# Kernel optimization log

Hardware: AMD Instinct MI355X
Metric: run time of the kernel (lower is better)

Reference implementation:

```python
import jax, jax.numpy as jnp
import numpy as np

FEAT_STRIDE = 16
POOL = 7
POST_NMS = 300
NUM_ANCHORS = 9
SCALES = np.array([8.0, 16.0, 32.0])
RATIOS = np.array([0.5, 1.0, 2.0])


def _base_anchors():
    w = h = 16.0
    xc = yc = 7.5
    size = w * h
    ws = np.round(np.sqrt(size / RATIOS))
    hs = np.round(ws * RATIOS)
    ratio_anchors = np.stack([xc - 0.5 * (ws - 1), yc - 0.5 * (hs - 1),
                              xc + 0.5 * (ws - 1), yc + 0.5 * (hs - 1)], 1)
    out = []
    for a in ratio_anchors:
        aw = a[2] - a[0] + 1.0
        ah = a[3] - a[1] + 1.0
        acx = a[0] + 0.5 * (aw - 1)
        acy = a[1] + 0.5 * (ah - 1)
        ws_ = aw * SCALES
        hs_ = ah * SCALES
        out.append(np.stack([acx - 0.5 * (ws_ - 1), acy - 0.5 * (hs_ - 1),
                             acx + 0.5 * (ws_ - 1), acy + 0.5 * (hs_ - 1)], 1))
    return np.concatenate(out, 0)  # [9,4]


def _all_anchors(H, W):
    base = _base_anchors()
    sx = np.arange(W) * FEAT_STRIDE
    sy = np.arange(H) * FEAT_STRIDE
    gx, gy = np.meshgrid(sx, sy)  # [H,W], x fastest -> matches NHWC flatten
    shifts = np.stack([gx.ravel(), gy.ravel(), gx.ravel(), gy.ravel()], 1)
    return jnp.asarray((shifts[:, None, :] + base[None, :, :]).reshape(-1, 4),
                       jnp.float32)  # [H*W*9, 4]


def _conv(x, w, b, pad):
    y = jax.lax.conv_general_dilated(x, w, (1, 1), [(pad, pad), (pad, pad)],
                                     dimension_numbers=('NCHW', 'OIHW', 'NCHW'))
    return y + b[None, :, None, None]


def _affine_grid(theta, H, W):
    # torch affine_grid, align_corners=True (torch<=1.2 default)
    xs = jnp.linspace(-1.0, 1.0, W)
    ys = jnp.linspace(-1.0, 1.0, H)
    gx, gy = jnp.meshgrid(xs, ys)
    base = jnp.stack([gx, gy, jnp.ones_like(gx)], -1)  # [H,W,3]
    return jnp.einsum('nij,hwj->nhwi', theta, base)  # [N,H,W,2] (x,y)


def _bilinear(img, x, y):
    # img [C,H,W]; x,y [h,w] pixel coords; zeros padding, align_corners=True
    H, W = img.shape[1], img.shape[2]
    x0 = jnp.floor(x)
    y0 = jnp.floor(y)
    x1 = x0 + 1.0
    y1 = y0 + 1.0
    wx1 = x - x0
    wx0 = 1.0 - wx1
    wy1 = y - y0
    wy0 = 1.0 - wy1

    def g(xi, yi):
        xc = jnp.clip(xi, 0, W - 1).astype(jnp.int32)
        yc = jnp.clip(yi, 0, H - 1).astype(jnp.int32)
        valid = ((xi >= 0) & (xi <= W - 1) & (yi >= 0) & (yi <= H - 1))
        return img[:, yc, xc] * valid.astype(img.dtype)

    return (g(x0, y0) * (wx0 * wy0) + g(x1, y0) * (wx1 * wy0)
            + g(x0, y1) * (wx0 * wy1) + g(x1, y1) * (wx1 * wy1))


def _pix(grid, H, W):
    x = (grid[..., 0] + 1.0) * 0.5 * (W - 1)
    y = (grid[..., 1] + 1.0) * 0.5 * (H - 1)
    return x, y


def strpn_forward(head_features, im_info, w_rpn, b_rpn, w_cls, b_cls,
                  w_bbox, b_bbox, w_trans, b_trans):
    H, W = head_features.shape[2], head_features.shape[3]
    anchors = _all_anchors(H, W)

    rpn = jax.nn.relu(_conv(head_features, w_rpn, b_rpn, 1))
    cls = _conv(rpn, w_cls, b_cls, 0)      # [1,18,H,W]
    bbox = _conv(rpn, w_bbox, b_bbox, 0)   # [1,36,H,W]
    trans = _conv(rpn, w_trans, b_trans, 0)  # [1,54,H,W]

    # view(1,2,9*H,W) softmax over dim1: channels 0..8=bg, 9..17=fg
    prob = jax.nn.softmax(cls.reshape(1, 2, NUM_ANCHORS, H, W), axis=1)[:, 1]
    scores = prob.transpose(0, 2, 3, 1).reshape(-1)          # [H*W*9]
    deltas = bbox.transpose(0, 2, 3, 1).reshape(-1, 4)
    tparam = trans.transpose(0, 2, 3, 1).reshape(-1, 6)

    # bbox_transform_inv
    aw = anchors[:, 2] - anchors[:, 0] + 1.0
    ah = anchors[:, 3] - anchors[:, 1] + 1.0
    acx = anchors[:, 0] + 0.5 * aw
    acy = anchors[:, 1] + 0.5 * ah
    pcx = deltas[:, 0] * aw + acx
    pcy = deltas[:, 1] * ah + acy
    pw = jnp.exp(deltas[:, 2]) * aw
    ph = jnp.exp(deltas[:, 3]) * ah
    x1 = jnp.clip(pcx - 0.5 * pw, 0.0, im_info[1] - 1.0)
    y1 = jnp.clip(pcy - 0.5 * ph, 0.0, im_info[0] - 1.0)
    x2 = jnp.clip(pcx + 0.5 * pw, 0.0, im_info[1] - 1.0)
    y2 = jnp.clip(pcy + 0.5 * ph, 0.0, im_info[0] - 1.0)

    # proposal selection: fixed-size top-K by fg score (NMS elided, see notes)
    _, idx = jax.lax.top_k(scores, POST_NMS)
    boxes = jnp.stack([x1, y1, x2, y2], 1)[idx]              # [300,4]
    tsel = tparam[idx]                                       # [300,6]
    rois = jnp.concatenate(
        [jnp.zeros((POST_NMS, 1), boxes.dtype), boxes], 1)   # [300,5]

    # affine-grid ROI pooling (STRPN.pooling, max_pool=True)
    fx1 = boxes[:, 0] / 16.0
    fy1 = boxes[:, 1] / 16.0
    fx2 = boxes[:, 2] / 16.0
    fy2 = boxes[:, 3] / 16.0
    Wf = jnp.float32(W)
    Hf = jnp.float32(H)
    t00 = (fx2 - fx1) / (Wf - 1)
    t02 = (fx1 + fx2 - Wf + 1) / (Wf - 1)
    t11 = (fy2 - fy1) / (Hf - 1)
    t12 = (fy1 + fy2 - Hf + 1) / (Hf - 1)
    z = jnp.zeros_like(t00)
    theta = jnp.stack([jnp.stack([t00, z, t02], -1),
                       jnp.stack([z, t11, t12], -1)], 1)     # [300,2,3]

    pre = 2 * POOL
    grid = _affine_grid(theta, pre, pre)
    xg, yg = _pix(grid, H, W)
    img = head_features[0]
    crops = jax.vmap(_bilinear, in_axes=(None, 0, 0))(img, xg, yg)  # [300,C,14,14]
    N, C = crops.shape[0], crops.shape[1]
    pooled = crops.reshape(N, C, POOL, 2, POOL, 2).max(axis=(3, 5))  # [300,C,7,7]

    # spatial transform with predicted per-ROI affine params
    theta2 = tsel.reshape(-1, 2, 3)
    grid2 = _affine_grid(theta2, POOL, POOL)
    x2g, y2g = _pix(grid2, POOL, POOL)
    transformed = jax.vmap(_bilinear)(pooled, x2g, y2g)       # [300,C,7,7]
    return rois, pooled, transformed


def setup_inputs() -> dict:
    key = jax.random.key(0)
    ks = jax.random.split(key, 10)
    C_in, C_rpn = 1024, 512
    inp = {
        'head_features': jax.random.normal(ks[0], (1, C_in, 50, 75), jnp.float32),
        'gt_boxes': jax.random.uniform(ks[1], (5, 5), jnp.float32) * 100.0,
        'im_info': jnp.array([800.0, 1200.0, 1.0], jnp.float32),
        'w_rpn': jax.random.normal(ks[2], (C_rpn, C_in, 3, 3), jnp.float32) * 0.01,
        'b_rpn': jnp.zeros((C_rpn,), jnp.float32),
        'w_cls': jax.random.normal(ks[3], (2 * NUM_ANCHORS, C_rpn, 1, 1), jnp.float32) * 0.01,
        'b_cls': jnp.zeros((2 * NUM_ANCHORS,), jnp.float32),
        'w_bbox': jax.random.normal(ks[4], (4 * NUM_ANCHORS, C_rpn, 1, 1), jnp.float32) * 0.01,
        'b_bbox': jnp.zeros((4 * NUM_ANCHORS,), jnp.float32),
        'w_trans': jax.random.normal(ks[5], (6 * NUM_ANCHORS, C_rpn, 1, 1), jnp.float32) * 0.01,
        'b_trans': jnp.zeros((6 * NUM_ANCHORS,), jnp.float32),
    }
    return inp


def reference(head_features, gt_boxes, im_info, w_rpn, b_rpn, w_cls, b_cls,
              w_bbox, b_bbox, w_trans, b_trans):
    # gt_boxes is unused in the inference 'gallery' path (kept for signature parity)
    return strpn_forward(head_features, im_info, w_rpn, b_rpn, w_cls, b_cls,
                         w_bbox, b_bbox, w_trans, b_trans)
```

## Files before the change

### kernel.cpp

```cpp
#include <hip/hip_runtime.h>
#include <hip/hip_bf16.h>
#include <stdint.h>

typedef unsigned int u32;
typedef unsigned long long u64;

#define HH 50
#define WW 75
#define NPOS 3750
#define NANCH 33750
#define CAP 4096
#define RPSZ 1920000

__constant__ float c_aw[9] = {184.f,368.f,736.f,128.f,256.f,512.f,88.f,176.f,352.f};
__constant__ float c_ah[9] = {96.f,192.f,384.f,128.f,256.f,512.f,176.f,352.f,704.f};

__global__ __launch_bounds__(256) void k_tw2(const float* __restrict__ w, float* __restrict__ wTb) {
  __shared__ __align__(16) float T[72*129];
  int tile = blockIdx.x;
  int ch   = blockIdx.y;
  int ocb = tile >> 2, ks = tile & 3;
  int t = threadIdx.x;
  const float* src = w + (size_t)(ocb*128)*9216 + (size_t)(ks*256 + ch*8)*9;
  #pragma unroll
  for (int i = 0; i < 36; ++i) {
    int e = t + i*256;
    int oc = e / 72, f = e - oc*72;
    T[f*129 + oc] = src[(size_t)oc*9216 + f];
  }
  __syncthreads();
  float* dst = wTb + ((size_t)tile*32 + ch)*9216;
  #pragma unroll
  for (int i = 0; i < 9; ++i) {
    int j = t + i*256;
    int f = j >> 5, o4 = (j & 31)*4;
    float4 v = make_float4(T[f*129+o4], T[f*129+o4+1], T[f*129+o4+2], T[f*129+o4+3]);
    *(float4*)&dst[(size_t)j*4] = v;
  }
}

__global__ __launch_bounds__(256) void k_tf(const float* __restrict__ head, float* __restrict__ fT) {
  __shared__ float tile[32][33];
  int p0 = blockIdx.x*32, c0 = blockIdx.y*32;
  int tx = threadIdx.x & 31, ty = threadIdx.x >> 5;
  #pragma unroll
  for (int k = 0; k < 4; ++k) {
    int cc = c0 + ty + k*8, pp = p0 + tx;
    tile[ty + k*8][tx] = (pp < NPOS) ? head[(size_t)cc*NPOS + pp] : 0.f;
  }
  __syncthreads();
  #pragma unroll
  for (int k = 0; k < 4; ++k) {
    int pp = p0 + ty + k*8, cc = c0 + tx;
    if (pp < NPOS) fT[(size_t)pp*1024 + cc] = tile[tx][ty + k*8];
  }
}

__global__ __launch_bounds__(256) void k_conv(const float* __restrict__ head,
                                              const float* __restrict__ wTb,
                                              float* __restrict__ rpnP) {
  __shared__ __align__(16) float Ws[9216];
  __shared__ __align__(16) float Xs[8*6*80 + 16];
  int ocb = blockIdx.x;
  int ks  = blockIdx.z;
  int t = threadIdx.x;
  int lane = t & 63;
  int g = blockIdx.y*4 + (t >> 6);
  if (g >= 125) g = 124;
  int rp  = __builtin_amdgcn_readfirstlane(g / 5);
  int sub = __builtin_amdgcn_readfirstlane(g - (g/5)*5);
  int rpA = (int)((blockIdx.y*4) / 5);
  int x0 = sub * 16;
  int rbase = 2*rpA - 1;
  int rloc = 2*(rp - rpA);

  float a00[16], a01[16], a10[16], a11[16];
  #pragma unroll
  for (int j = 0; j < 16; ++j) { a00[j]=0.f; a01[j]=0.f; a10[j]=0.f; a11[j]=0.f; }

  const float* wsrc = wTb + (size_t)(ocb*4 + ks)*32*9216;
  int ic0 = ks*256;

  #pragma unroll 1
  for (int ch = 0; ch < 32; ++ch) {
    #pragma unroll
    for (int i = 0; i < 9; ++i) {
      int e = t + i*256;
      *(float4*)&Ws[e*4] = *(const float4*)(wsrc + (size_t)ch*9216 + (size_t)e*4);
    }
    int icc = ic0 + ch*8;
    #pragma unroll
    for (int i = 0; i < 15; ++i) {
      int e = t + i*256;
      int il = e / 480; int r = e - il*480;
      int rr = r / 80;  int xx = r - rr*80;
      int sy = rbase + rr, sx = xx - 1;
      float v = 0.f;
      if (sy >= 0 && sy < HH && sx >= 0 && sx < WW)
        v = head[(size_t)(icc + il)*NPOS + sy*WW + sx];
      Xs[e] = v;
    }
    __syncthreads();
    #pragma unroll 1
    for (int il = 0; il < 8; ++il) {
      float wv0[9], wv1[9];
      #pragma unroll
      for (int k = 0; k < 9; ++k) {
        float2 w2 = *(const float2*)&Ws[(il*9 + k)*128 + 2*lane];
        wv0[k] = w2.x; wv1[k] = w2.y;
      }
      const float* xbase = &Xs[(il*6 + rloc)*80 + x0];
      #pragma unroll
      for (int ri = 0; ri < 4; ++ri) {
        float4 q0 = *(const float4*)(xbase + ri*80);
        float4 q1 = *(const float4*)(xbase + ri*80 + 4);
        float4 q2 = *(const float4*)(xbase + ri*80 + 8);
        float4 q3 = *(const float4*)(xbase + ri*80 + 12);
        float4 q4 = *(const float4*)(xbase + ri*80 + 16);
        float sxv[20] = {q0.x,q0.y,q0.z,q0.w, q1.x,q1.y,q1.z,q1.w,
                         q2.x,q2.y,q2.z,q2.w, q3.x,q3.y,q3.z,q3.w,
                         q4.x,q4.y,q4.z,q4.w};
        if (ri < 3) {
          #pragma unroll
          for (int kx = 0; kx < 3; ++kx) {
            float w0 = wv0[ri*3+kx], w1 = wv1[ri*3+kx];
            #pragma unroll
            for (int j = 0; j < 16; ++j) {
              a00[j] = fmaf(w0, sxv[j+kx], a00[j]);
              a01[j] = fmaf(w1, sxv[j+kx], a01[j]);
            }
          }
        }
        if (ri > 0) {
          #pragma unroll
          for (int kx = 0; kx < 3; ++kx) {
            float w0 = wv0[(ri-1)*3+kx], w1 = wv1[(ri-1)*3+kx];
            #pragma unroll
            for (int j = 0; j < 16; ++j) {
              a10[j] = fmaf(w0, sxv[j+kx], a10[j]);
              a11[j] = fmaf(w1, sxv[j+kx], a11[j]);
            }
          }
        }
      }
    }
    __syncthreads();
  }
  float* outp = rpnP + (size_t)ks*RPSZ;
  int ocl = ocb*128 + 2*lane;
  int or0 = 2*rp;
  #pragma unroll
  for (int j = 0; j < 16; ++j) {
    int x = x0 + j;
    if (x < WW) {
      *(float2*)&outp[(size_t)(or0*WW + x)*512 + ocl]     = make_float2(a00[j], a01[j]);
      *(float2*)&outp[(size_t)((or0+1)*WW + x)*512 + ocl] = make_float2(a10[j], a11[j]);
    }
  }
}

__global__ __launch_bounds__(256) void k_cls(const float* __restrict__ rp,
    const float* __restrict__ brpn,
    const float* __restrict__ w_cls, const float* __restrict__ b_cls,
    const float* __restrict__ w_bbox, const float* __restrict__ b_bbox,
    const float* __restrict__ w_tr, const float* __restrict__ b_tr,
    const float* __restrict__ iminfo,
    u32* __restrict__ sk, float* __restrict__ boxes, float* __restrict__ tpar) {
  __shared__ __align__(16) float R[128*68];
  __shared__ float O[16][112];
  int p0 = blockIdx.x << 4;
  int t = threadIdx.x;
  for (int e = t; e < 8192; e += 256) {
    int pos = e >> 9, ic = e & 511;
    int p = p0 + pos;
    float v = 0.f;
    if (p < NPOS) {
      size_t off = (size_t)p*512 + ic;
      v = rp[off] + rp[off + RPSZ] + rp[off + 2*(size_t)RPSZ] + rp[off + 3*(size_t)RPSZ] + brpn[ic];
      v = fmaxf(v, 0.f);
    }
    R[(ic>>2)*68 + pos*4 + (ic&3)] = v;
  }
  __syncthreads();
  int og = t >> 4, pos = t & 15;
  float acc[7];
  const float* wp[7];
  #pragma unroll
  for (int k = 0; k < 7; ++k) {
    acc[k] = 0.f;
    int o = og + (k << 4);
    if (o < 18)       wp[k] = w_cls + (size_t)o*512;
    else if (o < 54)  wp[k] = w_bbox + (size_t)(o-18)*512;
    else if (o < 108) wp[k] = w_tr + (size_t)(o-54)*512;
    else              wp[k] = w_cls;
  }
  for (int icg = 0; icg < 128; ++icg) {
    float4 xv = *(const float4*)&R[icg*68 + pos*4];
    #pragma unroll
    for (int k = 0; k < 7; ++k) {
      float4 wv = *(const float4*)(wp[k] + icg*4);
      acc[k] = fmaf(xv.x, wv.x, acc[k]);
      acc[k] = fmaf(xv.y, wv.y, acc[k]);
      acc[k] = fmaf(xv.z, wv.z, acc[k]);
      acc[k] = fmaf(xv.w, wv.w, acc[k]);
    }
  }
  #pragma unroll
  for (int k = 0; k < 7; ++k) {
    int o = og + (k << 4);
    if (o < 108) {
      float bv = (o < 18) ? b_cls[o] : (o < 54) ? b_bbox[o-18] : b_tr[o-54];
      O[pos][o] = acc[k] + bv;
    }
  }
  __syncthreads();
  if (t < 144) {
    int ps = t / 9, a = t - ps*9;
    int p = p0 + ps;
    if (p < NPOS) {
      int i = p*9 + a;
      float d = O[ps][9+a] - O[ps][a];
      float prob = 1.f / (1.f + expf(-d));
      u32 u = __float_as_uint(prob);
      sk[i] = (u & 0x80000000u) ? ~u : (u | 0x80000000u);
      int y = p / WW, x = p - y*WW;
      float aw = c_aw[a], ah = c_ah[a];
      float acx = x*16.f + 8.f, acy = y*16.f + 8.f;
      float dx = O[ps][18+a*4], dyv = O[ps][18+a*4+1], dz = O[ps][18+a*4+2], dw = O[ps][18+a*4+3];
      float pcx = dx*aw + acx, pcy = dyv*ah + acy;
      float pw = expf(dz)*aw, ph = expf(dw)*ah;
      float imh = iminfo[0], imw = iminfo[1];
      float x1 = fminf(fmaxf(pcx - 0.5f*pw, 0.f), imw - 1.f);
      float y1 = fminf(fmaxf(pcy - 0.5f*ph, 0.f), imh - 1.f);
      float x2 = fminf(fmaxf(pcx + 0.5f*pw, 0.f), imw - 1.f);
      float y2 = fminf(fmaxf(pcy + 0.5f*ph, 0.f), imh - 1.f);
      *(float4*)(boxes + (size_t)i*4) = make_float4(x1,y1,x2,y2);
      #pragma unroll
      for (int j = 0; j < 6; ++j) tpar[(size_t)i*6 + j] = O[ps][54 + a*6 + j];
    }
  }
}

__global__ __launch_bounds__(256) void k_hist(const u32* __restrict__ sk, u32* __restrict__ hist) {
  int i = blockIdx.x*256 + threadIdx.x;
  if (i < NANCH) atomicAdd(&hist[sk[i] >> 16], 1u);
}

__global__ __launch_bounds__(1024) void k_thresh(const u32* __restrict__ hist, u32* __restrict__ thr) {
  __shared__ u32 S[1024];
  __shared__ int tstar;
  int t = threadIdx.x;
  u32 s = 0;
  for (int j = 0; j < 64; ++j) s += hist[t*64 + j];
  S[t] = s;
  __syncthreads();
  for (int d = 1; d < 1024; d <<= 1) {
    u32 v = (t + d < 1024) ? S[t + d] : 0;
    __syncthreads();
    S[t] += v;
    __syncthreads();
  }
  if (S[t] >= 300 && (t == 1023 || S[t+1] < 300)) tstar = t;
  __syncthreads();
  if (t == 0) {
    int ts = tstar;
    u32 c = (ts < 1023) ? S[ts+1] : 0;
    int T = ts*64;
    for (int b = ts*64 + 63; b >= ts*64; --b) {
      c += hist[b];
      if (c >= 300) { T = b; break; }
    }
    thr[0] = (u32)T;
  }
}

__global__ __launch_bounds__(256) void k_compact(const u32* __restrict__ sk, const u32* __restrict__ thr,
                                                 u64* __restrict__ cand, u32* __restrict__ cnt) {
  int i = blockIdx.x*256 + threadIdx.x;
  if (i >= NANCH) return;
  u32 k = sk[i];
  if ((k >> 16) >= thr[0]) {
    u32 p = atomicAdd(cnt, 1u);
    if (p < CAP) cand[p] = ((u64)k << 32) | (u32)(~(u32)i);
  }
}

__global__ __launch_bounds__(1024) void k_sortsel(const u64* __restrict__ cand, const u32* __restrict__ cnt,
    const float* __restrict__ boxes, const float* __restrict__ tpar,
    float* __restrict__ out_rois, float* __restrict__ selb, float* __restrict__ selt) {
  __shared__ u64 A[CAP];
  int t = threadIdx.x;
  int n = min((int)cnt[0], CAP);
  for (int i = t; i < CAP; i += 1024) A[i] = (i < n) ? cand[i] : 0ull;
  __syncthreads();
  for (int k = 2; k <= CAP; k <<= 1) {
    for (int j = k >> 1; j > 0; j >>= 1) {
      for (int i = t; i < CAP; i += 1024) {
        int p = i ^ j;
        if (p > i) {
          u64 a = A[i], b = A[p];
          bool dir = (i & k) == 0;
          if (dir ? (a < b) : (a > b)) { A[i] = b; A[p] = a; }
        }
      }
      __syncthreads();
    }
  }
  if (t < 300) {
    u32 idx = ~((u32)A[t]);
    float4 bx = *(const float4*)(boxes + (size_t)idx*4);
    out_rois[t*5+0] = 0.f;
    out_rois[t*5+1] = bx.x; out_rois[t*5+2] = bx.y;
    out_rois[t*5+3] = bx.z; out_rois[t*5+4] = bx.w;
    *(float4*)(selb + t*4) = bx;
    #pragma unroll
    for (int j = 0; j < 6; ++j) selt[t*6+j] = tpar[(size_t)idx*6 + j];
  }
}

__global__ __launch_bounds__(256) void k_pool(const float* __restrict__ fT,
    const float* __restrict__ selb, const float* __restrict__ selt,
    float* __restrict__ outP, float* __restrict__ outTr) {
  __shared__ __align__(16) float pl[256*49];
  int r = blockIdx.y;
  int c0 = blockIdx.x << 8;
  int t = threadIdx.x;
  const float* img = fT + c0 + t;
  float bx1 = selb[r*4], by1 = selb[r*4+1], bx2 = selb[r*4+2], by2 = selb[r*4+3];
  float fx1 = bx1*0.0625f, fy1 = by1*0.0625f, fx2 = bx2*0.0625f, fy2 = by2*0.0625f;
  float t00 = (fx2-fx1)*(1.f/74.f);
  float t02 = (fx1+fx2-74.f)*(1.f/74.f);
  float t11 = (fy2-fy1)*(1.f/49.f);
  float t12 = (fy1+fy2-49.f)*(1.f/49.f);
  for (int py = 0; py < 7; ++py) {
    float m[7];
    #pragma unroll
    for (int q = 0; q < 7; ++q) m[q] = -3.4e38f;
    #pragma unroll
    for (int dy = 0; dy < 2; ++dy) {
      int sy = py*2 + dy;
      float gy = -1.f + sy*(2.f/13.f);
      float yf = (t11*gy + t12 + 1.f)*24.5f;
      float y0f = floorf(yf);
      float wy1 = yf - y0f, wy0 = 1.f - wy1;
      bool vy0 = (y0f >= 0.f && y0f <= 49.f);
      bool vy1 = (y0f >= -1.f && y0f <= 48.f);
      float yc = fminf(fmaxf(y0f, -2.f), 51.f);
      int iy0 = min(max((int)yc, 0), 49);
      int iy1 = min(max((int)yc + 1, 0), 49);
      #pragma unroll
      for (int sx = 0; sx < 14; ++sx) {
        float gx = -1.f + sx*(2.f/13.f);
        float xf = (t00*gx + t02 + 1.f)*37.f;
        float x0f = floorf(xf);
        float wx1 = xf - x0f, wx0 = 1.f - wx1;
        bool vx0 = (x0f >= 0.f && x0f <= 74.f);
        bool vx1 = (x0f >= -1.f && x0f <= 73.f);
        float xc = fminf(fmaxf(x0f, -2.f), 76.f);
        int ix0 = min(max((int)xc, 0), 74);
        int ix1 = min(max((int)xc + 1, 0), 74);
        float v00 = (vx0 && vy0) ? img[(size_t)(iy0*WW + ix0)*1024] : 0.f;
        float v10 = (vx1 && vy0) ? img[(size_t)(iy0*WW + ix1)*1024] : 0.f;
        float v01 = (vx0 && vy1) ? img[(size_t)(iy1*WW + ix0)*1024] : 0.f;
        float v11 = (vx1 && vy1) ? img[(size_t)(iy1*WW + ix1)*1024] : 0.f;
        float val = v00*(wx0*wy0) + v10*(wx1*wy0) + v01*(wx0*wy1) + v11*(wx1*wy1);
        m[sx>>1] = fmaxf(m[sx>>1], val);
      }
    }
    #pragma unroll
    for (int q = 0; q < 7; ++q) pl[t*49 + py*7 + q] = m[q];
  }
  __syncthreads();
  size_t base = (size_t)r*50176 + (size_t)c0*49;
  for (int jj = t; jj < 3136; jj += 256)
    *(float4*)(outP + base + (size_t)jj*4) = *(const float4*)&pl[jj*4];
  float T0 = selt[r*6], T1 = selt[r*6+1], T2 = selt[r*6+2];
  float T3 = selt[r*6+3], T4 = selt[r*6+4], T5 = selt[r*6+5];
  float tr[49];
  #pragma unroll
  for (int qy = 0; qy < 7; ++qy) {
    float gy = -1.f + qy*(1.f/3.f);
    #pragma unroll
    for (int qx = 0; qx < 7; ++qx) {
      float gx = -1.f + qx*(1.f/3.f);
      float xf = (T0*gx + T1*gy + T2 + 1.f)*3.f;
      float yf = (T3*gx + T4*gy + T5 + 1.f)*3.f;
      float x0f = floorf(xf), y0f = floorf(yf);
      float wx1 = xf - x0f, wx0 = 1.f - wx1;
      float wy1 = yf - y0f, wy0 = 1.f - wy1;
      bool vx0 = (x0f >= 0.f && x0f <= 6.f), vx1 = (x0f >= -1.f && x0f <= 5.f);
      bool vy0 = (y0f >= 0.f && y0f <= 6.f), vy1 = (y0f >= -1.f && y0f <= 5.f);
      float xc = fminf(fmaxf(x0f, -2.f), 8.f);
      float ycl = fminf(fmaxf(y0f, -2.f), 8.f);
      int ix0 = min(max((int)xc, 0), 6), ix1 = min(max((int)xc + 1, 0), 6);
      int iy0 = min(max((int)ycl, 0), 6), iy1 = min(max((int)ycl + 1, 0), 6);
      const float* P = &pl[t*49];
      float v00 = (vx0&&vy0) ? P[iy0*7+ix0] : 0.f;
      float v10 = (vx1&&vy0) ? P[iy0*7+ix1] : 0.f;
      float v01 = (vx0&&vy1) ? P[iy1*7+ix0] : 0.f;
      float v11 = (vx1&&vy1) ? P[iy1*7+ix1] : 0.f;
      tr[qy*7+qx] = v00*(wx0*wy0) + v10*(wx1*wy0) + v01*(wx0*wy1) + v11*(wx1*wy1);
    }
  }
  __syncthreads();
  #pragma unroll
  for (int q = 0; q < 49; ++q) pl[t*49 + q] = tr[q];
  __syncthreads();
  for (int jj = t; jj < 3136; jj += 256)
    *(float4*)(outTr + base + (size_t)jj*4) = *(const float4*)&pl[jj*4];
}

extern "C" void kernel_launch(void* const* d_in, const int* in_sizes, int n_in,
                              void* d_out, int out_size, void* d_ws, size_t ws_size,
                              hipStream_t stream) {
  (void)in_sizes; (void)n_in; (void)out_size; (void)ws_size;
  const float* head   = (const float*)d_in[0];
  const float* iminfo = (const float*)d_in[2];
  const float* w_rpn  = (const float*)d_in[3];
  const float* b_rpn  = (const float*)d_in[4];
  const float* w_cls  = (const float*)d_in[5];
  const float* b_cls  = (const float*)d_in[6];
  const float* w_bbox = (const float*)d_in[7];
  const float* b_bbox = (const float*)d_in[8];
  const float* w_tr   = (const float*)d_in[9];
  const float* b_tr   = (const float*)d_in[10];
  float* out = (float*)d_out;
  float* out_rois = out;
  float* outP = out + 1500;
  float* outT = out + 1500 + 15052800;

  char* wsp = (char*)d_ws;
  size_t off = 0;
  auto alloc = [&](size_t bytes) -> void* {
    void* p = wsp + off;
    off = (off + bytes + 255) & ~(size_t)255;
    return p;
  };
  float* wTb   = (float*)alloc(4718592ull*4);
  float* rpnP  = (float*)alloc(4ull*RPSZ*4);
  u32*   sk    = (u32*)alloc(NANCH*4);
  float* boxes = (float*)alloc((size_t)NANCH*4*4);
  float* tpar  = (float*)alloc((size_t)NANCH*6*4);
  u32*   hist  = (u32*)alloc(65536*4);
  u32*   cnt   = (u32*)alloc(256);
  u64*   cand  = (u64*)alloc(CAP*8);
  float* selb  = (float*)alloc(300*4*4);
  float* selt  = (float*)alloc(300*6*4);
  float* fT    = wTb;

  hipMemsetAsync(hist, 0, 65536*4, stream);
  hipMemsetAsync(cnt, 0, 8, stream);

  k_tw2<<<dim3(16, 32), 256, 0, stream>>>(w_rpn, wTb);
  k_conv<<<dim3(4, 32, 4), 256, 0, stream>>>(head, wTb, rpnP);
  k_tf<<<dim3(118, 32), 256, 0, stream>>>(head, fT);
  k_cls<<<235, 256, 0, stream>>>(rpnP, b_rpn, w_cls, b_cls, w_bbox, b_bbox,
                                 w_tr, b_tr, iminfo, sk, boxes, tpar);
  k_hist<<<132, 256, 0, stream>>>(sk, hist);
  k_thresh<<<1, 1024, 0, stream>>>(hist, cnt + 1);
  k_compact<<<132, 256, 0, stream>>>(sk, cnt + 1, cand, cnt);
  k_sortsel<<<1, 1024, 0, stream>>>(cand, cnt, boxes, tpar, out_rois, selb, selt);
  k_pool<<<dim3(4, 300), 256, 0, stream>>>(fT, selb, selt, outP, outT);
}
```

Before: 947.0 us.

## Pre-pad conv input and double-buffer input tiles with register prefetch

A new kernel writes a zero-padded copy of the head features, so the conv no longer needs bounds checks and can load float4 chunks. The conv kernel is retiled so each block covers 8 output rows by 16 columns, one wave per row pair. Input tiles are double-buffered in LDS, with the next channel chunk prefetched into registers while the current one is computed, which removes one barrier per chunk. Weights are now read straight from global memory instead of being staged in LDS. This trades an extra pad pass and more cache-dependent weight traffic for fewer barriers and less LDS traffic.

```diff
diff --git a/kernel.cpp b/kernel.cpp
--- a/kernel.cpp
+++ b/kernel.cpp
@@ -39,6 +39,21 @@
   }
 }
 
+__global__ __launch_bounds__(256) void k_pad2(const float* __restrict__ head, float* __restrict__ hp) {
+  int T = blockIdx.x*256 + threadIdx.x;
+  int ic = T / 1218; int rem = T - ic*1218;
+  int r = rem / 21, c4 = rem - r*21;
+  int sy = r - 1;
+  float v[4];
+  #pragma unroll
+  for (int c = 0; c < 4; ++c) {
+    int sx = c4*4 + c - 1;
+    v[c] = (sy >= 0 && sy < HH && sx >= 0 && sx < WW)
+         ? head[(size_t)ic*NPOS + sy*WW + sx] : 0.f;
+  }
+  *(float4*)&hp[(size_t)T*4] = make_float4(v[0],v[1],v[2],v[3]);
+}
+
 __global__ __launch_bounds__(256) void k_tf(const float* __restrict__ head, float* __restrict__ fT) {
   __shared__ float tile[32][33];
   int p0 = blockIdx.x*32, c0 = blockIdx.y*32;
@@ -56,105 +71,114 @@
   }
 }
 
-__global__ __launch_bounds__(256) void k_conv(const float* __restrict__ head,
+__global__ __launch_bounds__(256) void k_conv(const float* __restrict__ hp,
                                               const float* __restrict__ wTb,
                                               float* __restrict__ rpnP) {
-  __shared__ __align__(16) float Ws[9216];
-  __shared__ __align__(16) float Xs[8*6*80 + 16];
+  __shared__ __align__(16) float Xs[2][1600];
   int ocb = blockIdx.x;
   int ks  = blockIdx.z;
-  int t = threadIdx.x;
-  int lane = t & 63;
-  int g = blockIdx.y*4 + (t >> 6);
-  if (g >= 125) g = 124;
-  int rp  = __builtin_amdgcn_readfirstlane(g / 5);
-  int sub = __builtin_amdgcn_readfirstlane(g - (g/5)*5);
-  int rpA = (int)((blockIdx.y*4) / 5);
-  int x0 = sub * 16;
-  int rbase = 2*rpA - 1;
-  int rloc = 2*(rp - rpA);
+  int g   = blockIdx.y;
+  int R   = g / 5, sub = g - (g/5)*5;
+  int t = threadIdx.x;
+  int w = t >> 6, lane = t & 63;
+  int or0 = __builtin_amdgcn_readfirstlane(8*R + 2*w);
+  bool awave = (or0 < HH);
+  int rloc = __builtin_amdgcn_readfirstlane(2*w);
+  int x0 = sub*16;
+
+  const float* wsrc = wTb + (size_t)(ocb*4 + ks)*32*9216 + 2*lane;
+  int ic0 = ks*256;
+
+  int f1 = t + 256;
+  bool has1 = f1 < 400;
+  int il0 = t/50,  r0 = (t%50)/5,  x40 = t%5;
+  int il1 = f1/50, r1 = (f1%50)/5, x41 = f1%5;
+  const float4* hp4 = (const float4*)hp;
+  size_t c0s = (size_t)(ic0 + il0)*1218 + (size_t)(8*R + r0)*21 + 4*sub + x40;
+  size_t c1s = (size_t)(ic0 + il1)*1218 + (size_t)(8*R + r1)*21 + 4*sub + x41;
+
+  float4 s0 = hp4[c0s];
+  float4 s1 = has1 ? hp4[c1s] : s0;
+  ((float4*)Xs[0])[t] = s0;
+  if (has1) ((float4*)Xs[0])[f1] = s1;
+  __syncthreads();
 
   float a00[16], a01[16], a10[16], a11[16];
   #pragma unroll
   for (int j = 0; j < 16; ++j) { a00[j]=0.f; a01[j]=0.f; a10[j]=0.f; a11[j]=0.f; }
-
-  const float* wsrc = wTb + (size_t)(ocb*4 + ks)*32*9216;
-  int ic0 = ks*256;
 
   #pragma unroll 1
   for (int ch = 0; ch < 32; ++ch) {
-    #pragma unroll
-    for (int i = 0; i < 9; ++i) {
-      int e = t + i*256;
-      *(float4*)&Ws[e*4] = *(const float4*)(wsrc + (size_t)ch*9216 + (size_t)e*4);
-    }
-    int icc = ic0 + ch*8;
-    #pragma unroll
-    for (int i = 0; i < 15; ++i) {
-      int e = t + i*256;
-      int il = e / 480; int r = e - il*480;
-      int rr = r / 80;  int xx = r - rr*80;
-      int sy = rbase + rr, sx = xx - 1;
-      float v = 0.f;
-      if (sy >= 0 && sy < HH && sx >= 0 && sx < WW)
-        v = head[(size_t)(icc + il)*NPOS + sy*WW + sx];
-      Xs[e] = v;
-    }
-    __syncthreads();
-    #pragma unroll 1
-    for (int il = 0; il < 8; ++il) {
-      float wv0[9], wv1[9];
-      #pragma unroll
-      for (int k = 0; k < 9; ++k) {
-        float2 w2 = *(const float2*)&Ws[(il*9 + k)*128 + 2*lane];
-        wv0[k] = w2.x; wv1[k] = w2.y;
-      }
-      const float* xbase = &Xs[(il*6 + rloc)*80 + x0];
-      #pragma unroll
-      for (int ri = 0; ri < 4; ++ri) {
-        float4 q0 = *(const float4*)(xbase + ri*80);
-        float4 q1 = *(const float4*)(xbase + ri*80 + 4);
-        float4 q2 = *(const float4*)(xbase + ri*80 + 8);
-        float4 q3 = *(const float4*)(xbase + ri*80 + 12);
-        float4 q4 = *(const float4*)(xbase + ri*80 + 16);
-        float sxv[20] = {q0.x,q0.y,q0.z,q0.w, q1.x,q1.y,q1.z,q1.w,
-                         q2.x,q2.y,q2.z,q2.w, q3.x,q3.y,q3.z,q3.w,
-                         q4.x,q4.y,q4.z,q4.w};
-        if (ri < 3) {
-          #pragma unroll
-          for (int kx = 0; kx < 3; ++kx) {
-            float w0 = wv0[ri*3+kx], w1 = wv1[ri*3+kx];
+    int cur = ch & 1;
+    if (ch < 31) {
+      size_t adv = (size_t)(ch+1)*8*1218;
+      s0 = hp4[c0s + adv];
+      if (has1) s1 = hp4[c1s + adv];
+    }
+    if (awave) {
+      const float* wch = wsrc + (size_t)ch*9216;
+      #pragma unroll 1
+      for (int il = 0; il < 8; ++il) {
+        float wv0[9], wv1[9];
+        #pragma unroll
+        for (int k = 0; k < 9; ++k) {
+          float2 w2 = *(const float2*)(wch + (il*9 + k)*128);
+          wv0[k] = w2.x; wv1[k] = w2.y;
+        }
+        const float* xb = &Xs[cur][il*200 + rloc*20 + x0/4*4];
+        #pragma unroll
+        for (int ri = 0; ri < 4; ++ri) {
+          const float* xr = &Xs[cur][il*200 + (rloc + ri)*20];
+          float4 q0 = *(const float4*)(xr + 0);
+          float4 q1 = *(const float4*)(xr + 4);
+          float4 q2 = *(const float4*)(xr + 8);
+          float4 q3 = *(const float4*)(xr + 12);
+          float4 q4 = *(const float4*)(xr + 16);
+          float xv[20] = {q0.x,q0.y,q0.z,q0.w, q1.x,q1.y,q1.z,q1.w,
+                          q2.x,q2.y,q2.z,q2.w, q3.x,q3.y,q3.z,q3.w,
+                          q4.x,q4.y,q4.z,q4.w};
+          if (ri < 3) {
             #pragma unroll
-            for (int j = 0; j < 16; ++j) {
-              a00[j] = fmaf(w0, sxv[j+kx], a00[j]);
-              a01[j] = fmaf(w1, sxv[j+kx], a01[j]);
+            for (int kx = 0; kx < 3; ++kx) {
+              float w0 = wv0[ri*3+kx], w1 = wv1[ri*3+kx];
+              #pragma unroll
+              for (int j = 0; j < 16; ++j) {
+                a00[j] = fmaf(w0, xv[j+kx], a00[j]);
+                a01[j] = fmaf(w1, xv[j+kx], a01[j]);
+              }
             }
           }
-        }
-        if (ri > 0) {
-          #pragma unroll
-          for (int kx = 0; kx < 3; ++kx) {
-            float w0 = wv0[(ri-1)*3+kx], w1 = wv1[(ri-1)*3+kx];
+          if (ri > 0) {
             #pragma unroll
-            for (int j = 0; j < 16; ++j) {
-              a10[j] = fmaf(w0, sxv[j+kx], a10[j]);
-              a11[j] = fmaf(w1, sxv[j+kx], a11[j]);
+            for (int kx = 0; kx < 3; ++kx) {
+              float w0 = wv0[(ri-1)*3+kx], w1 = wv1[(ri-1)*3+kx];
+              #pragma unroll
+              for (int j = 0; j < 16; ++j) {
+                a10[j] = fmaf(w0, xv[j+kx], a10[j]);
+                a11[j] = fmaf(w1, xv[j+kx], a11[j]);
+              }
             }
           }
         }
       }
     }
+    if (ch < 31) {
+      ((float4*)Xs[cur^1])[t] = s0;
+      if (has1) ((float4*)Xs[cur^1])[f1] = s1;
+    }
     __syncthreads();
   }
-  float* outp = rpnP + (size_t)ks*RPSZ;
-  int ocl = ocb*128 + 2*lane;
-  int or0 = 2*rp;
-  #pragma unroll
-  for (int j = 0; j < 16; ++j) {
-    int x = x0 + j;
-    if (x < WW) {
-      *(float2*)&outp[(size_t)(or0*WW + x)*512 + ocl]     = make_float2(a00[j], a01[j]);
-      *(float2*)&outp[(size_t)((or0+1)*WW + x)*512 + ocl] = make_float2(a10[j], a11[j]);
+
+  if (awave) {
+    float* outp = rpnP + (size_t)ks*RPSZ;
+    int ocl = ocb*128 + 2*lane;
+    #pragma unroll
+    for (int j = 0; j < 16; ++j) {
+      int x = x0 + j;
+      if (x < WW) {
+        *(float2*)&outp[(size_t)(or0*WW + x)*512 + ocl]       = make_float2(a00[j], a01[j]);
+        *(float2*)&outp[(size_t)((or0+1)*WW + x)*512 + ocl]   = make_float2(a10[j], a11[j]);
+      }
     }
   }
 }
@@ -437,6 +461,7 @@
     return p;
   };
   float* wTb   = (float*)alloc(4718592ull*4);
+  float* hp    = (float*)alloc(4988928ull*4);
   float* rpnP  = (float*)alloc(4ull*RPSZ*4);
   u32*   sk    = (u32*)alloc(NANCH*4);
   float* boxes = (float*)alloc((size_t)NANCH*4*4);
@@ -446,13 +471,14 @@
   u64*   cand  = (u64*)alloc(CAP*8);
   float* selb  = (float*)alloc(300*4*4);
   float* selt  = (float*)alloc(300*6*4);
-  float* fT    = wTb;
+  float* fT    = hp;
 
   hipMemsetAsync(hist, 0, 65536*4, stream);
   hipMemsetAsync(cnt, 0, 8, stream);
 
   k_tw2<<<dim3(16, 32), 256, 0, stream>>>(w_rpn, wTb);
-  k_conv<<<dim3(4, 32, 4), 256, 0, stream>>>(head, wTb, rpnP);
+  k_pad2<<<4872, 256, 0, stream>>>(head, hp);
+  k_conv<<<dim3(4, 35, 4), 256, 0, stream>>>(hp, wTb, rpnP);
   k_tf<<<dim3(118, 32), 256, 0, stream>>>(head, fT);
   k_cls<<<235, 256, 0, stream>>>(rpnP, b_rpn, w_cls, b_cls, w_bbox, b_bbox,
                                  w_tr, b_tr, iminfo, sk, boxes, tpar);
```

Measured after the change: 1.120 ms. +18.3%, slower.
